# Kernel tuning notes

Measured on AMD Instinct MI355X. Metric: run time of the kernel, lower is better.

## Reference

```python
import jax, jax.numpy as jnp
import numpy as np

B, T, H = 8, 2048, 1024
P = 64           # num_attention_project
N = 4096         # config.n (bias table length), N >= 2T-1
WINDOW = 64      # relative_attention
NEG = -10000.0


def setup_inputs() -> dict:
    key = jax.random.key(0)
    ks = jax.random.split(key, 10)
    s = 1.0 / np.sqrt(H)
    sp = 1.0 / np.sqrt(P)
    sb = 1.0 / np.sqrt(N)
    return {
        "attn_input": jax.random.normal(ks[0], (B, T, H), dtype=jnp.float32),
        "attention_mask": jnp.ones((B, T), dtype=jnp.float32),
        # Linear weights stored as [in, out] so y = x @ W + b
        "Wq": jax.random.uniform(ks[1], (H, P), minval=-s, maxval=s),
        "bq": jnp.zeros((P,), jnp.float32),
        "Wk": jax.random.uniform(ks[2], (H, P), minval=-s, maxval=s),
        "bk": jnp.zeros((P,), jnp.float32),
        "Wv": jax.random.uniform(ks[3], (H, P), minval=-s, maxval=s),
        "bv": jnp.zeros((P,), jnp.float32),
        "Wo": jax.random.uniform(ks[4], (P, H), minval=-sp, maxval=sp),
        "bo": jnp.zeros((H,), jnp.float32),
        "bias": jax.random.uniform(ks[5], (N,), minval=-sb, maxval=sb),
    }


def reference(attn_input, attention_mask, Wq, bq, Wk, bk, Wv, bv, Wo, bo, bias):
    q = attn_input @ Wq + bq            # [B,T,P]
    k = attn_input @ Wk + bk
    v = attn_input @ Wv + bv
    scores = jnp.einsum("btp,bsp->bts", q, k) / jnp.sqrt(jnp.float32(P))  # [B,T,T]
    # padding mask: note original broadcasts over COLUMNS via unsqueeze(-1)
    scores = scores + (1.0 - attention_mask)[:, :, None] * NEG
    # circulant window mask: keep |i-j| <= WINDOW (all ones if WINDOW >= T)
    i = jnp.arange(T)
    rel = i[:, None] - i[None, :]       # i - j
    win = (jnp.abs(rel) <= WINDOW) | (WINDOW >= T)
    scores = scores + jnp.where(win, 0.0, NEG)[None, :, :]
    # gathered learnable relative-position bias: bias[n//2 - i + j]
    scores = scores + bias[N // 2 - rel][None, :, :]
    attn = jax.nn.softmax(scores, axis=-1)
    out = jnp.einsum("bts,bsp->btp", attn, v)
    return out @ Wo + bo                # [B,T,H]
```

## Files before the change

kernel.cpp:

```cpp
#include <hip/hip_runtime.h>

using bf16x8 = __attribute__((ext_vector_type(8))) short;
using f32x4  = __attribute__((ext_vector_type(4))) float;

static __device__ inline unsigned short f2bf(float f) {
  unsigned int u = __float_as_uint(f);
  u += 0x7fffu + ((u >> 16) & 1u);
  return (unsigned short)(u >> 16);
}
static __device__ inline unsigned int pk2(float a, float b) {
  return (unsigned int)f2bf(a) | ((unsigned int)f2bf(b) << 16);
}

#define BAR_LGKM() { asm volatile("s_waitcnt lgkmcnt(0)" ::: "memory"); \
                     __builtin_amdgcn_sched_barrier(0); \
                     __builtin_amdgcn_s_barrier(); }

#define ROW16_MAX(x) { \
  { int _t = __builtin_amdgcn_update_dpp(0, __float_as_int(x), 0x121, 0xf, 0xf, true); x = fmaxf(x, __int_as_float(_t)); } \
  { int _t = __builtin_amdgcn_update_dpp(0, __float_as_int(x), 0x122, 0xf, 0xf, true); x = fmaxf(x, __int_as_float(_t)); } \
  { int _t = __builtin_amdgcn_update_dpp(0, __float_as_int(x), 0x124, 0xf, 0xf, true); x = fmaxf(x, __int_as_float(_t)); } \
  { int _t = __builtin_amdgcn_update_dpp(0, __float_as_int(x), 0x128, 0xf, 0xf, true); x = fmaxf(x, __int_as_float(_t)); } }
#define ROW16_SUM(x) { \
  { int _t = __builtin_amdgcn_update_dpp(0, __float_as_int(x), 0x121, 0xf, 0xf, true); x += __int_as_float(_t); } \
  { int _t = __builtin_amdgcn_update_dpp(0, __float_as_int(x), 0x122, 0xf, 0xf, true); x += __int_as_float(_t); } \
  { int _t = __builtin_amdgcn_update_dpp(0, __float_as_int(x), 0x124, 0xf, 0xf, true); x += __int_as_float(_t); } \
  { int _t = __builtin_amdgcn_update_dpp(0, __float_as_int(x), 0x128, 0xf, 0xf, true); x += __int_as_float(_t); } }

__global__ __launch_bounds__(256) void prep_kernel(
    const float* __restrict__ Wq, const float* __restrict__ Wk, const float* __restrict__ Wv,
    const float* __restrict__ Wo, const float* __restrict__ bq, const float* __restrict__ bk,
    const float* __restrict__ bv,
    unsigned short* __restrict__ Wt, unsigned short* __restrict__ Wot, float* __restrict__ bqkv)
{
  int idx = blockIdx.x * 256 + threadIdx.x;
  if (idx < 192 * 1024) {
    int n = idx >> 10, k = idx & 1023;
    const float* W = (n < 64) ? Wq : (n < 128) ? Wk : Wv;
    Wt[idx] = f2bf(W[k * 64 + (n & 63)]);
  } else if (idx < 192 * 1024 + 1024 * 64) {
    int j = idx - 192 * 1024;
    int n = j >> 6, k = j & 63;
    Wot[j] = f2bf(Wo[k * 1024 + n]);
  } else if (idx < 192 * 1024 + 1024 * 64 + 192) {
    int n = idx - (192 * 1024 + 1024 * 64);
    bqkv[n] = (n < 64) ? bq[n] : (n < 128) ? bk[n - 64] : bv[n - 128];
  }
}

__global__ __launch_bounds__(1024, 4) void fused_attn(
    const float* __restrict__ X, const unsigned short* __restrict__ Wt,
    const float* __restrict__ bqkv, const float* __restrict__ bias,
    const unsigned short* __restrict__ Wot, const float* __restrict__ bo,
    float* __restrict__ out)
{
  __shared__ __align__(16) char smem[113664];
  unsigned short* const Kl  = (unsigned short*)(smem);
  unsigned short* const Vt  = (unsigned short*)(smem + 27648);
  unsigned short* const PsU = (unsigned short*)(smem + 55296);
  float* const Mx    = (float*)(smem + 110592);
  float* const Lx    = (float*)(smem + 111616);
  float* const biasL = (float*)(smem + 112640);
  unsigned short* const As_ = (unsigned short*)(smem);
  unsigned short* const Bs_ = (unsigned short*)(smem + 55296);

  int t = threadIdx.x;
  int lane = t & 63, w = t >> 6;
  int col = lane & 15, quad = lane >> 4, q4 = quad * 4;
  int L = ((blockIdx.x & 7) << 5) | (blockIdx.x >> 3);
  int b = L >> 5;
  int i0 = (L & 31) * 64;
  const float* xbase = X + (size_t)(b << 11) * 1024;

  if (t < 129) biasL[t] = bias[1984 + t];

  int wm = w >> 2, wn = w & 3;
  f32x4 acc[3][3] = {};
  int tr = t >> 4, c4 = t & 15;
  int offA[3], offB[3];
  #pragma unroll
  for (int i = 0; i < 3; ++i) {
    int row = i * 64 + tr;
    int jb = i0 - 64 + row;
    int jc = jb < 0 ? 0 : (jb > 2047 ? 2047 : jb);
    offA[i] = jc * 1024 + c4 * 4;
    offB[i] = row * 1024 + c4 * 4;
  }
  float bov[3];
  #pragma unroll
  for (int nt = 0; nt < 3; ++nt) bov[nt] = bqkv[wn * 48 + nt * 16 + col];

  float4 pA[3]; uint2 pB[3];
  #pragma unroll
  for (int i = 0; i < 3; ++i) {
    pA[i] = *(const float4*)(xbase + offA[i]);
    pB[i] = *(const uint2*)(Wt + offB[i]);
  }
  for (int ks = 0; ks < 16; ++ks) {
    unsigned short* A  = As_ + (ks & 1) * 13824;
    unsigned short* Bb = Bs_ + (ks & 1) * 13824;
    #pragma unroll
    for (int i = 0; i < 3; ++i) {
      *(uint2*)(A  + (i * 64 + tr) * 72 + c4 * 4) =
          make_uint2(pk2(pA[i].x, pA[i].y), pk2(pA[i].z, pA[i].w));
      *(uint2*)(Bb + (i * 64 + tr) * 72 + c4 * 4) = pB[i];
    }
    if (ks + 1 < 16) {
      #pragma unroll
      for (int i = 0; i < 3; ++i) {
        pA[i] = *(const float4*)(xbase + offA[i] + (ks + 1) * 64);
        pB[i] = *(const uint2*)(Wt + offB[i] + (ks + 1) * 64);
      }
    }
    BAR_LGKM();
    #pragma unroll
    for (int kk = 0; kk < 64; kk += 32) {
      int ko = kk + quad * 8;
      bf16x8 bfr[3];
      #pragma unroll
      for (int nt = 0; nt < 3; ++nt)
        bfr[nt] = *(const bf16x8*)(Bb + ((wn * 3 + nt) * 16 + col) * 72 + ko);
      #pragma unroll
      for (int mt = 0; mt < 3; ++mt) {
        bf16x8 afr = *(const bf16x8*)(A + ((wm * 3 + mt) * 16 + col) * 72 + ko);
        #pragma unroll
        for (int nt = 0; nt < 3; ++nt)
          acc[mt][nt] = __builtin_amdgcn_mfma_f32_16x16x32_bf16(afr, bfr[nt], acc[mt][nt], 0, 0, 0);
      }
    }
  }
  BAR_LGKM();

  #pragma unroll
  for (int mt = 0; mt < 3; ++mt) {
    #pragma unroll
    for (int nt = 0; nt < 3; ++nt) {
      int n = wn * 48 + nt * 16 + col;
      #pragma unroll
      for (int r = 0; r < 4; ++r) {
        int m = wm * 48 + mt * 16 + q4 + r;
        unsigned short h = f2bf(acc[mt][nt][r] + bov[nt]);
        if (n < 64) {
          if (m >= 64 && m < 128) PsU[(m - 64) * 72 + n] = h;
        } else if (n < 128) {
          Kl[m * 72 + (n - 64)] = h;
        } else {
          Vt[(n - 128) * 216 + m] = h;
        }
      }
    }
  }
  if (t < 256) {
    int pz = t >> 2, c0 = 192 + (t & 3) * 4;
    *(uint2*)(Vt + pz * 216 + c0) = make_uint2(0u, 0u);
  }
  BAR_LGKM();

  int g = w >> 2, u = w & 3;
  int iq = i0 + g * 16;
  bf16x8 aq0 = *(const bf16x8*)(PsU + (g * 16 + col) * 72 + quad * 8);
  bf16x8 aq1 = *(const bf16x8*)(PsU + (g * 16 + col) * 72 + 32 + quad * 8);

  int nt9 = (u == 0) ? 3 : 2;
  int t9b = (u == 0) ? 0 : (2 * u + 1);
  f32x4 sv[3];
  for (int i = 0; i < nt9; ++i) {
    int t9 = t9b + i;
    int krow = ((g + t9) * 16 + col) * 72;
    bf16x8 kb0 = *(const bf16x8*)(Kl + krow + quad * 8);
    bf16x8 kb1 = *(const bf16x8*)(Kl + krow + 32 + quad * 8);
    f32x4 z = {};
    z = __builtin_amdgcn_mfma_f32_16x16x32_bf16(aq0, kb0, z, 0, 0, 0);
    sv[i] = __builtin_amdgcn_mfma_f32_16x16x32_bf16(aq1, kb1, z, 0, 0, 0);
  }
  float mrow[4] = {-3e38f, -3e38f, -3e38f, -3e38f};
  for (int i = 0; i < nt9; ++i) {
    int t9 = t9b + i;
    int j = iq - 64 + t9 * 16 + col;
    #pragma unroll
    for (int r = 0; r < 4; ++r) {
      int diff = q4 + r + 64 - t9 * 16 - col;
      bool valid = (j >= 0) & (j < 2048) & (diff >= -64) & (diff <= 64);
      int bi = 64 - diff; bi = bi < 0 ? 0 : (bi > 128 ? 128 : bi);
      float x = valid ? (sv[i][r] * 0.125f + biasL[bi]) : -3e38f;
      sv[i][r] = x;
      mrow[r] = fmaxf(mrow[r], x);
    }
  }
  #pragma unroll
  for (int r = 0; r < 4; ++r) ROW16_MAX(mrow[r]);
  if (col == 0) {
    #pragma unroll
    for (int r = 0; r < 4; ++r) Mx[w * 16 + q4 + r] = mrow[r];
  }
  BAR_LGKM();
  #pragma unroll
  for (int r = 0; r < 4; ++r) {
    float m0_ = Mx[(g * 4 + 0) * 16 + q4 + r];
    float m1_ = Mx[(g * 4 + 1) * 16 + q4 + r];
    float m2_ = Mx[(g * 4 + 2) * 16 + q4 + r];
    float m3_ = Mx[(g * 4 + 3) * 16 + q4 + r];
    mrow[r] = fmaxf(fmaxf(m0_, m1_), fmaxf(m2_, m3_));
  }

  unsigned short* Pw = PsU + g * 2688;
  float lsum[4] = {0.f, 0.f, 0.f, 0.f};
  for (int i = 0; i < nt9; ++i) {
    int t9 = t9b + i;
    #pragma unroll
    for (int r = 0; r < 4; ++r) {
      float pe = __expf(sv[i][r] - mrow[r]);
      lsum[r] += pe;
      Pw[(q4 + r) * 168 + t9 * 16 + col] = f2bf(pe);
    }
  }
  #pragma unroll
  for (int r = 0; r < 4; ++r) ROW16_SUM(lsum[r]);
  if (col == 0) {
    #pragma unroll
    for (int r = 0; r < 4; ++r) Lx[w * 16 + q4 + r] = lsum[r];
  }
  if (u == 0) {
    #pragma unroll
    for (int r = 0; r < 4; ++r) Pw[(q4 + r) * 168 + 144 + col] = 0;
  }
  BAR_LGKM();
  #pragma unroll
  for (int r = 0; r < 4; ++r)
    lsum[r] = Lx[(g * 4 + 0) * 16 + q4 + r] + Lx[(g * 4 + 1) * 16 + q4 + r]
            + Lx[(g * 4 + 2) * 16 + q4 + r] + Lx[(g * 4 + 3) * 16 + q4 + r];

  f32x4 o = {};
  #pragma unroll
  for (int kc = 0; kc < 5; ++kc) {
    bf16x8 pa = *(const bf16x8*)(Pw + col * 168 + kc * 32 + quad * 8);
    bf16x8 vb = *(const bf16x8*)(Vt + (u * 16 + col) * 216 + g * 16 + kc * 32 + quad * 8);
    o = __builtin_amdgcn_mfma_f32_16x16x32_bf16(pa, vb, o, 0, 0, 0);
  }
  BAR_LGKM();
  {
    float rl[4];
    #pragma unroll
    for (int r = 0; r < 4; ++r) rl[r] = 1.0f / lsum[r];
    #pragma unroll
    for (int r = 0; r < 4; ++r)
      PsU[(g * 16 + q4 + r) * 72 + u * 16 + col] = f2bf(o[r] * rl[r]);
  }
  BAR_LGKM();

  int n0 = w * 64;
  const unsigned short* wb_base = Wot + (size_t)(n0 + col) * 64 + quad * 8;
  bf16x8 wb[4][2];
  #pragma unroll
  for (int ns = 0; ns < 4; ++ns) {
    wb[ns][0] = *(const bf16x8*)(wb_base + ns * 16 * 64);
    wb[ns][1] = *(const bf16x8*)(wb_base + ns * 16 * 64 + 32);
  }
  float bov4[4];
  #pragma unroll
  for (int ns = 0; ns < 4; ++ns) bov4[ns] = bo[n0 + ns * 16 + col];
  float* outbase = out + ((size_t)(b << 11) + i0) * 1024 + n0;
  #pragma unroll
  for (int mt = 0; mt < 4; ++mt) {
    bf16x8 a0 = *(const bf16x8*)(PsU + (mt * 16 + col) * 72 + quad * 8);
    bf16x8 a1 = *(const bf16x8*)(PsU + (mt * 16 + col) * 72 + 32 + quad * 8);
    f32x4 a4[4] = {};
    #pragma unroll
    for (int ns = 0; ns < 4; ++ns) {
      a4[ns] = __builtin_amdgcn_mfma_f32_16x16x32_bf16(a0, wb[ns][0], a4[ns], 0, 0, 0);
      a4[ns] = __builtin_amdgcn_mfma_f32_16x16x32_bf16(a1, wb[ns][1], a4[ns], 0, 0, 0);
    }
    #pragma unroll
    for (int ns = 0; ns < 4; ++ns)
      #pragma unroll
      for (int r = 0; r < 4; ++r)
        outbase[(size_t)(mt * 16 + q4 + r) * 1024 + ns * 16 + col] = a4[ns][r] + bov4[ns];
  }
}

extern "C" void kernel_launch(void* const* d_in, const int* in_sizes, int n_in,
                              void* d_out, int out_size, void* d_ws, size_t ws_size,
                              hipStream_t stream) {
  const float* X    = (const float*)d_in[0];
  const float* Wq   = (const float*)d_in[2];
  const float* bq   = (const float*)d_in[3];
  const float* Wk   = (const float*)d_in[4];
  const float* bk   = (const float*)d_in[5];
  const float* Wv   = (const float*)d_in[6];
  const float* bv   = (const float*)d_in[7];
  const float* Wo   = (const float*)d_in[8];
  const float* bo   = (const float*)d_in[9];
  const float* bias = (const float*)d_in[10];
  float* out = (float*)d_out;
  char* ws = (char*)d_ws;
  unsigned short* Wt   = (unsigned short*)(ws);
  unsigned short* Wot  = (unsigned short*)(ws + 393216);
  float*          bqkv = (float*)(ws + 524288);

  prep_kernel<<<1025, 256, 0, stream>>>(Wq, Wk, Wv, Wo, bq, bk, bv, Wt, Wot, bqkv);
  fused_attn<<<256, 1024, 0, stream>>>(X, Wt, bqkv, bias, Wot, bo, out);
}
```

Measured before the change: 159.5 us.

## Deepen QKV projection prefetch to two stages, raise MFMA priority, hoist Wo loads

The QKV projection loop is unrolled by two with two register prefetch sets, so global loads for step ks+2 and ks+3 are in flight while the current step's MFMAs run. The MFMA section is wrapped in s_setprio to favour matrix issue. The V-transpose store is packed into one 8-byte write per fragment instead of four scalar stores, and the Wo fragment and bias loads are moved up so their latency is hidden behind attention. The cost is more live registers under the 1024-thread launch bound, which may cause spills.

```diff
diff --git a/kernel.cpp b/kernel.cpp
--- a/kernel.cpp
+++ b/kernel.cpp
@@ -48,6 +48,38 @@
   }
 }
 
+
+#define P1_LOAD(KS, PA, PB) { \
+  _Pragma("unroll") \
+  for (int i_ = 0; i_ < 3; ++i_) { \
+    PA[i_] = *(const float4*)(xbase + offA[i_] + (KS) * 64); \
+    PB[i_] = *(const uint2*)(Wt + offB[i_] + (KS) * 64); } }
+
+#define P1_STORE(AB, BB, PA, PB) { \
+  _Pragma("unroll") \
+  for (int i_ = 0; i_ < 3; ++i_) { \
+    *(uint2*)((AB) + (i_ * 64 + tr) * 72 + c4 * 4) = \
+        make_uint2(pk2(PA[i_].x, PA[i_].y), pk2(PA[i_].z, PA[i_].w)); \
+    *(uint2*)((BB) + (i_ * 64 + tr) * 72 + c4 * 4) = PB[i_]; } }
+
+#define P1_MMA(AB, BB) { \
+  __builtin_amdgcn_s_setprio(1); \
+  _Pragma("unroll") \
+  for (int kk = 0; kk < 64; kk += 32) { \
+    int ko = kk + quad * 8; \
+    bf16x8 bfr[3]; \
+    _Pragma("unroll") \
+    for (int nt = 0; nt < 3; ++nt) \
+      bfr[nt] = *(const bf16x8*)((BB) + ((wn * 3 + nt) * 16 + col) * 72 + ko); \
+    _Pragma("unroll") \
+    for (int mt = 0; mt < 3; ++mt) { \
+      bf16x8 afr = *(const bf16x8*)((AB) + ((wm * 3 + mt) * 16 + col) * 72 + ko); \
+      _Pragma("unroll") \
+      for (int nt = 0; nt < 3; ++nt) \
+        acc[mt][nt] = __builtin_amdgcn_mfma_f32_16x16x32_bf16(afr, bfr[nt], acc[mt][nt], 0, 0, 0); \
+    } } \
+  __builtin_amdgcn_s_setprio(0); }
+
 __global__ __launch_bounds__(1024, 4) void fused_attn(
     const float* __restrict__ X, const unsigned short* __restrict__ Wt,
     const float* __restrict__ bqkv, const float* __restrict__ bias,
@@ -90,63 +122,56 @@
   #pragma unroll
   for (int nt = 0; nt < 3; ++nt) bov[nt] = bqkv[wn * 48 + nt * 16 + col];
 
-  float4 pA[3]; uint2 pB[3];
-  #pragma unroll
-  for (int i = 0; i < 3; ++i) {
-    pA[i] = *(const float4*)(xbase + offA[i]);
-    pB[i] = *(const uint2*)(Wt + offB[i]);
-  }
-  for (int ks = 0; ks < 16; ++ks) {
-    unsigned short* A  = As_ + (ks & 1) * 13824;
-    unsigned short* Bb = Bs_ + (ks & 1) * 13824;
-    #pragma unroll
-    for (int i = 0; i < 3; ++i) {
-      *(uint2*)(A  + (i * 64 + tr) * 72 + c4 * 4) =
-          make_uint2(pk2(pA[i].x, pA[i].y), pk2(pA[i].z, pA[i].w));
-      *(uint2*)(Bb + (i * 64 + tr) * 72 + c4 * 4) = pB[i];
-    }
-    if (ks + 1 < 16) {
-      #pragma unroll
-      for (int i = 0; i < 3; ++i) {
-        pA[i] = *(const float4*)(xbase + offA[i] + (ks + 1) * 64);
-        pB[i] = *(const uint2*)(Wt + offB[i] + (ks + 1) * 64);
-      }
-    }
+  float4 pA0[3], pA1[3]; uint2 pB0[3], pB1[3];
+  P1_LOAD(0, pA0, pB0);
+  P1_LOAD(1, pA1, pB1);
+  unsigned short* const A0 = As_;            unsigned short* const B0 = Bs_;
+  unsigned short* const A1 = As_ + 13824;    unsigned short* const B1 = Bs_ + 13824;
+  for (int ks = 0; ks < 16; ks += 2) {
+    P1_STORE(A0, B0, pA0, pB0);
+    if (ks + 2 < 16) P1_LOAD(ks + 2, pA0, pB0);
     BAR_LGKM();
-    #pragma unroll
-    for (int kk = 0; kk < 64; kk += 32) {
-      int ko = kk + quad * 8;
-      bf16x8 bfr[3];
-      #pragma unroll
-      for (int nt = 0; nt < 3; ++nt)
-        bfr[nt] = *(const bf16x8*)(Bb + ((wn * 3 + nt) * 16 + col) * 72 + ko);
-      #pragma unroll
-      for (int mt = 0; mt < 3; ++mt) {
-        bf16x8 afr = *(const bf16x8*)(A + ((wm * 3 + mt) * 16 + col) * 72 + ko);
-        #pragma unroll
-        for (int nt = 0; nt < 3; ++nt)
-          acc[mt][nt] = __builtin_amdgcn_mfma_f32_16x16x32_bf16(afr, bfr[nt], acc[mt][nt], 0, 0, 0);
-      }
-    }
-  }
-  BAR_LGKM();
+    P1_MMA(A0, B0);
+    P1_STORE(A1, B1, pA1, pB1);
+    if (ks + 3 < 16) P1_LOAD(ks + 3, pA1, pB1);
+    BAR_LGKM();
+    P1_MMA(A1, B1);
+  }
+  BAR_LGKM();
+
+  int n0 = w * 64;
+  const unsigned short* wb_base = Wot + (size_t)(n0 + col) * 64 + quad * 8;
+  bf16x8 wb[4][2];
+  #pragma unroll
+  for (int ns = 0; ns < 4; ++ns) {
+    wb[ns][0] = *(const bf16x8*)(wb_base + ns * 16 * 64);
+    wb[ns][1] = *(const bf16x8*)(wb_base + ns * 16 * 64 + 32);
+  }
+  float bov4[4];
+  #pragma unroll
+  for (int ns = 0; ns < 4; ++ns) bov4[ns] = bo[n0 + ns * 16 + col];
 
   #pragma unroll
   for (int mt = 0; mt < 3; ++mt) {
     #pragma unroll
     for (int nt = 0; nt < 3; ++nt) {
       int n = wn * 48 + nt * 16 + col;
-      #pragma unroll
-      for (int r = 0; r < 4; ++r) {
-        int m = wm * 48 + mt * 16 + q4 + r;
-        unsigned short h = f2bf(acc[mt][nt][r] + bov[nt]);
-        if (n < 64) {
-          if (m >= 64 && m < 128) PsU[(m - 64) * 72 + n] = h;
-        } else if (n < 128) {
-          Kl[m * 72 + (n - 64)] = h;
-        } else {
-          Vt[(n - 128) * 216 + m] = h;
+      int mbase = wm * 48 + mt * 16 + q4;
+      if (n < 64) {
+        #pragma unroll
+        for (int r = 0; r < 4; ++r) {
+          int m = mbase + r;
+          if (m >= 64 && m < 128) PsU[(m - 64) * 72 + n] = f2bf(acc[mt][nt][r] + bov[nt]);
         }
+      } else if (n < 128) {
+        #pragma unroll
+        for (int r = 0; r < 4; ++r)
+          Kl[(mbase + r) * 72 + (n - 64)] = f2bf(acc[mt][nt][r] + bov[nt]);
+      } else {
+        uint2 pv = make_uint2(
+            pk2(acc[mt][nt][0] + bov[nt], acc[mt][nt][1] + bov[nt]),
+            pk2(acc[mt][nt][2] + bov[nt], acc[mt][nt][3] + bov[nt]));
+        *(uint2*)(Vt + (n - 128) * 216 + mbase) = pv;
       }
     }
   }
@@ -248,17 +273,6 @@
   }
   BAR_LGKM();
 
-  int n0 = w * 64;
-  const unsigned short* wb_base = Wot + (size_t)(n0 + col) * 64 + quad * 8;
-  bf16x8 wb[4][2];
-  #pragma unroll
-  for (int ns = 0; ns < 4; ++ns) {
-    wb[ns][0] = *(const bf16x8*)(wb_base + ns * 16 * 64);
-    wb[ns][1] = *(const bf16x8*)(wb_base + ns * 16 * 64 + 32);
-  }
-  float bov4[4];
-  #pragma unroll
-  for (int ns = 0; ns < 4; ++ns) bov4[ns] = bo[n0 + ns * 16 + col];
   float* outbase = out + ((size_t)(b << 11) + i0) * 1024 + n0;
   #pragma unroll
   for (int mt = 0; mt < 4; ++mt) {
```

Result: slower. 211.0 us (+32.3%).
